# Performance work log

Hardware: AMD Instinct MI355X
Metric: run time of the kernel (lower is better)

The kernel has to match this reference:

```python
import jax, jax.numpy as jnp
import numpy as np

MB = 512          # mini_batch_size from init
BETA = 0.5        # RKHSMatrixOptimizer beta
N_SIGMAS = 50     # forward calls sigma_optimizer.step(..., 50)
EPS = 1e-6        # epsilon added to eigenvalues


def _pdist2(a):
    # squared Euclidean pairwise distances, matches torch.cdist(a, a)**2
    sq = jnp.sum(a * a, axis=1)
    d2 = sq[:, None] + sq[None, :] - 2.0 * (a @ a.T)
    return jnp.maximum(d2, 0.0)


def _rbf(d2, sigma):
    return jnp.exp(-d2 / (sigma ** 2))


def _entropy(A):
    # matrix-based Renyi entropy: eigh, +eps, -sum(w log2 w)
    w = jnp.linalg.eigvalsh(A) + EPS
    return -jnp.sum(w * jnp.log2(w))


def _joint_entropy(Ax, Ay):
    aux = Ax * Ay
    return _entropy(aux / jnp.trace(aux))


def _mi(Ax, Ay):
    return _entropy(Ax) + _entropy(Ay) - _joint_entropy(Ax, Ay)


def setup_inputs() -> dict:
    key = jax.random.key(0)
    k1, k2, k3 = jax.random.split(key, 3)
    x = jax.random.normal(k1, (4096, 8192), dtype=jnp.float32)
    inp = jax.random.normal(k2, (4096, 3, 32, 32), dtype=jnp.float32)
    label = jax.random.uniform(k3, (4096, 10), dtype=jnp.float32)
    return {"x": x, "input": inp, "label": label}


def reference(x, input, label):
    xf = x.reshape(x.shape[0], -1)
    inpf = input.reshape(input.shape[0], -1)
    n_batches = xf.shape[0] // MB

    sigma = None
    Ixt, Ity = [], []
    for b in range(n_batches):
        sl = slice(b * MB, (b + 1) * MB)
        xb, ib, lb = xf[sl], inpf[sl], label[sl]
        n = xb.shape[0]

        # label kernel Ky = RBF(label_batch, 0.1)
        Ky = _rbf(_pdist2(lb), 0.1)

        # sigma search: compute pairwise distances ONCE, broadcast over 50 sigmas
        d2 = _pdist2(xb)
        d = jnp.sqrt(d2)
        mean_d = jnp.sum(d) / jnp.maximum(jnp.sum(d2 > 0), 1)  # mean of nonzero dists
        start = 0.1 * mean_d
        step = (10.0 * mean_d - start) / N_SIGMAS
        sigmas = start + step * jnp.arange(N_SIGMAS, dtype=jnp.float32)  # np.arange equiv
        Ks = jnp.exp(-d2[None, :, :] / (sigmas[:, None, None] ** 2))  # [50, n, n]
        num = jnp.sum(Ks * Ky[None], axis=(1, 2))
        den = jnp.sqrt(jnp.sum(Ks * Ks, axis=(1, 2))) * jnp.linalg.norm(Ky)
        loss = num / den  # kernel alignment
        sigma_t = sigmas[jnp.argmax(loss)]
        sigma = sigma_t if sigma is None else BETA * sigma + (1.0 - BETA) * sigma_t

        # normalized Gram matrices (tensorRBFMatrix divides by batch size)
        A = _rbf(d2, sigma) / n
        Ay = Ky / n
        Ax = _rbf(_pdist2(ib), 8.0) / n

        Ixt.append(_mi(Ax, A))
        Ity.append(_mi(A, Ay))

    Ixt_mean = jnp.mean(jnp.stack(Ixt))
    Ity_mean = jnp.mean(jnp.stack(Ity))
    # torch forward returns x unchanged; MI values are stored as side effects.
    return x, Ixt_mean, Ity_mean
```

## Files before the change

kernel.cpp:

```cpp
#include <hip/hip_runtime.h>
#include <hip/hip_bf16.h>
#include <math.h>


#define NBATCH 8
#define MBS    512
#define DXX    8192
#define DII    3072
#define NSIG   50
#define NN     262144
#define NTOT   ((size_t)33554432)

#define I_SUMD  0
#define I_KYF   8
#define I_SIGMA 24
#define I_ENT   32
#define I_NUM   96
#define I_DEN   512
#define I_AX2   912
#define I_A2    920
#define I_JX2   928
#define I_JY2   936

typedef __attribute__((ext_vector_type(8))) short bf16x8;
typedef __attribute__((ext_vector_type(4))) float f32x4;

__device__ __forceinline__ size_t slotOf(int b, int m) {
  return ((size_t)(b * 5 + m)) * (size_t)NN;
}

__device__ __forceinline__ short f2b(float f) {
  __hip_bfloat16 h = __float2bfloat16(f);
  return *(short*)&h;
}

__device__ __forceinline__ ushort4 cvt4(float4 a) {
  ushort4 v;
  v.x = (ushort)f2b(a.x); v.y = (ushort)f2b(a.y);
  v.z = (ushort)f2b(a.z); v.w = (ushort)f2b(a.w);
  return v;
}

__device__ __forceinline__ double n4(float4 a) {
  return (double)a.x * a.x + (double)a.y * a.y + (double)a.z * a.z + (double)a.w * a.w;
}

__device__ __forceinline__ void nt_store4(float4 v, float4* p) {
  f32x4 w = {v.x, v.y, v.z, v.w};
  __builtin_nontemporal_store(w, (f32x4*)p);
}

__global__ void k_copy(const float4* __restrict__ src, float4* __restrict__ dst, size_t n4) {
  size_t i = (size_t)blockIdx.x * blockDim.x + threadIdx.x;
  size_t stride = (size_t)gridDim.x * blockDim.x;
  for (; i < n4; i += stride) dst[i] = src[i];
}

__global__ __launch_bounds__(256) void k_prep(
    const float4* __restrict__ x4, float4* __restrict__ xcopy, int docopy,
    const float* __restrict__ inp, const float* __restrict__ lab,
    ushort* __restrict__ xbf, ushort* __restrict__ inpbf,
    float* __restrict__ nrmx, float* __restrict__ nrmi,
    float* __restrict__ eig, double* __restrict__ scal)
{
  __shared__ double red[256];
  int bid = blockIdx.x, t = threadIdx.x;

  if (bid < 4096) {
    int row = bid;
    const float4* p4 = x4 + (size_t)row * 2048;
    float4 f0 = p4[t];
    float4 f1 = p4[t + 256];
    float4 f2 = p4[t + 512];
    float4 f3 = p4[t + 768];
    float4 f4 = p4[t + 1024];
    float4 f5 = p4[t + 1280];
    float4 f6 = p4[t + 1536];
    float4 f7 = p4[t + 1792];
    if (docopy) {
      float4* q4 = xcopy + (size_t)row * 2048;
      nt_store4(f0, q4 + t);
      nt_store4(f1, q4 + t + 256);
      nt_store4(f2, q4 + t + 512);
      nt_store4(f3, q4 + t + 768);
      nt_store4(f4, q4 + t + 1024);
      nt_store4(f5, q4 + t + 1280);
      nt_store4(f6, q4 + t + 1536);
      nt_store4(f7, q4 + t + 1792);
    }
    ushort4* o4 = (ushort4*)(xbf + (size_t)row * 8192);
    o4[t]        = cvt4(f0);
    o4[t + 256]  = cvt4(f1);
    o4[t + 512]  = cvt4(f2);
    o4[t + 768]  = cvt4(f3);
    o4[t + 1024] = cvt4(f4);
    o4[t + 1280] = cvt4(f5);
    o4[t + 1536] = cvt4(f6);
    o4[t + 1792] = cvt4(f7);
    double s = n4(f0) + n4(f1) + n4(f2) + n4(f3) + n4(f4) + n4(f5) + n4(f6) + n4(f7);
    red[t] = s; __syncthreads();
    for (int o2 = 128; o2 > 0; o2 >>= 1) {
      if (t < o2) red[t] += red[t + o2];
      __syncthreads();
    }
    if (t == 0) nrmx[row] = (float)red[0];
    return;
  }

  if (bid < 6144) {
    int p = bid - 4096;
    const float4* src4 = (const float4*)inp + (size_t)p * 768;
    ushort4* dst4 = (ushort4*)inpbf + (size_t)p * 768;
    float4 g0 = src4[t];
    float4 g1 = src4[t + 256];
    float4 g2 = src4[t + 512];
    dst4[t]       = cvt4(g0);
    dst4[t + 256] = cvt4(g1);
    dst4[t + 512] = cvt4(g2);
    double s0 = n4(g0), s1 = n4(g2);
    double sm = n4(g1);
    if (t < 128) s0 += sm; else s1 += sm;
    red[t] = s0; __syncthreads();
    for (int o = 128; o > 0; o >>= 1) { if (t < o) red[t] += red[t + o]; __syncthreads(); }
    if (t == 0) nrmi[2 * p] = (float)red[0];
    __syncthreads();
    red[t] = s1; __syncthreads();
    for (int o = 128; o > 0; o >>= 1) { if (t < o) red[t] += red[t + o]; __syncthreads(); }
    if (t == 0) nrmi[2 * p + 1] = (float)red[0];
    return;
  }

  int idx = bid - 6144;
  int b = idx >> 8, xb = idx & 255;
  int e0 = xb * 1024 + t * 4;
  int i = e0 >> 9;
  const float* L = lab + (size_t)b * MBS * 10;
  float4 out;
  double s = 0.0;
#pragma unroll
  for (int u = 0; u < 4; u++) {
    int j = (e0 & 511) + u;
    float d2 = 0.0f;
#pragma unroll
    for (int d = 0; d < 10; d++) { float dd = L[i * 10 + d] - L[j * 10 + d]; d2 += dd * dd; }
    float ky = __expf(-d2 * 100.0f);
    ((float*)&out)[u] = ky * (1.0f / 512.0f);
    s += (double)ky * ky;
  }
  *(float4*)&eig[slotOf(b, 2) + e0] = out;
  red[t] = s; __syncthreads();
  for (int o = 128; o > 0; o >>= 1) { if (t < o) red[t] += red[t + o]; __syncthreads(); }
  if (t == 0) atomicAdd(&scal[I_KYF + b], red[0]);
}

#define LSTR 72
#define LGKM0_BAR                                                             \
  do {                                                                        \
    asm volatile("s_waitcnt lgkmcnt(0)" ::: "memory");                        \
    __builtin_amdgcn_s_barrier();                                             \
    __builtin_amdgcn_sched_barrier(0);                                        \
  } while (0)

#define LOAD_SET(A0, A1, B0, B1, K0)                                          \
  do {                                                                        \
    A0 = *(const bf16x8*)&srcA0[K0];                                          \
    A1 = *(const bf16x8*)&srcA1[K0];                                          \
    B0 = *(const bf16x8*)&srcB0[K0];                                          \
    B1 = *(const bf16x8*)&srcB1[K0];                                          \
  } while (0)

#define WRITE_LDS(BUF, A0, A1, B0, B1)                                        \
  do {                                                                        \
    *(bf16x8*)&As[BUF][rr * LSTR + cc] = A0;                                  \
    *(bf16x8*)&As[BUF][(32 + rr) * LSTR + cc] = A1;                           \
    *(bf16x8*)&Bs[BUF][rr * LSTR + cc] = B0;                                  \
    *(bf16x8*)&Bs[BUF][(32 + rr) * LSTR + cc] = B1;                           \
  } while (0)

#define MFMA_PHASE(BUF)                                                       \
  do {                                                                        \
    _Pragma("unroll")                                                         \
    for (int ks = 0; ks < 2; ks++) {                                          \
      bf16x8 af0 = *(const bf16x8*)&As[BUF][(wr + l15) * LSTR + ks * 32 + l4 * 8];          \
      bf16x8 af1 = *(const bf16x8*)&As[BUF][(wr + 16 + l15) * LSTR + ks * 32 + l4 * 8];     \
      bf16x8 bg0 = *(const bf16x8*)&Bs[BUF][(wc + l15) * LSTR + ks * 32 + l4 * 8];          \
      bf16x8 bg1 = *(const bf16x8*)&Bs[BUF][(wc + 16 + l15) * LSTR + ks * 32 + l4 * 8];     \
      acc00 = __builtin_amdgcn_mfma_f32_16x16x32_bf16(af0, bg0, acc00, 0, 0, 0);            \
      acc01 = __builtin_amdgcn_mfma_f32_16x16x32_bf16(af0, bg1, acc01, 0, 0, 0);            \
      acc10 = __builtin_amdgcn_mfma_f32_16x16x32_bf16(af1, bg0, acc10, 0, 0, 0);            \
      acc11 = __builtin_amdgcn_mfma_f32_16x16x32_bf16(af1, bg1, acc11, 0, 0, 0);            \
    }                                                                         \
  } while (0)

__global__ __launch_bounds__(256) void k_gemm2(
    const ushort* __restrict__ xbf, const ushort* __restrict__ inpbf,
    const float* __restrict__ nrmx, const float* __restrict__ nrmi,
    float* __restrict__ eig, double* __restrict__ scal,
    unsigned long long* __restrict__ cnt)
{
  int id = blockIdx.x;
  int b = id & 7;
  int tm = id >> 3;
  int mode = (tm >= 36) ? 1 : 0;
  int t = tm - mode * 36;
  int bx = 0;
#pragma unroll
  for (int r = 1; r < 8; r++) if (t >= (r * (r + 1)) / 2) bx = r;
  int by = t - (bx * (bx + 1)) / 2;
  bool diag = (bx == by);
  int D = mode ? DII : DXX;
  const ushort* src = (mode ? inpbf : xbf) + (size_t)b * MBS * D;
  const float* nb = (mode ? nrmi : nrmx) + b * MBS;
  int row0 = bx * 64, col0 = by * 64;

  __shared__ ushort As[2][64 * LSTR];
  __shared__ ushort Bs[2][64 * LSTR];
  __shared__ double redd[256];
  __shared__ unsigned redi[256];

  int tid = threadIdx.x;
  int lane = tid & 63, w = tid >> 6;
  int wr = (w >> 1) * 32, wc = (w & 1) * 32;
  int l15 = lane & 15, l4 = lane >> 4;

  f32x4 acc00 = {0.f, 0.f, 0.f, 0.f}, acc01 = {0.f, 0.f, 0.f, 0.f};
  f32x4 acc10 = {0.f, 0.f, 0.f, 0.f}, acc11 = {0.f, 0.f, 0.f, 0.f};

  int rr = tid >> 3;
  int cc = (tid & 7) * 8;

  const ushort* srcA0 = src + (size_t)(row0 + rr) * D + cc;
  const ushort* srcA1 = src + (size_t)(row0 + 32 + rr) * D + cc;
  const ushort* srcB0 = src + (size_t)(col0 + rr) * D + cc;
  const ushort* srcB1 = src + (size_t)(col0 + 32 + rr) * D + cc;

  bf16x8 pa0, pa1, pb0, pb1;
  bf16x8 qa0, qa1, qb0, qb1;

  LOAD_SET(pa0, pa1, pb0, pb1, 0);
  LOAD_SET(qa0, qa1, qb0, qb1, 64);

  int nk = D >> 6;
  for (int k = 0; k < nk; k += 2) {
    WRITE_LDS(0, pa0, pa1, pb0, pb1);
    if (k + 2 < nk) LOAD_SET(pa0, pa1, pb0, pb1, (k + 2) << 6);
    LGKM0_BAR;
    MFMA_PHASE(0);
    WRITE_LDS(1, qa0, qa1, qb0, qb1);
    if (k + 3 < nk) LOAD_SET(qa0, qa1, qb0, qb1, (k + 3) << 6);
    LGKM0_BAR;
    MFMA_PHASE(1);
  }

  float* dst = eig + slotOf(b, mode ? 0 : 1);
  double lsum = 0.0; unsigned lcnt = 0;
#define EPI(ACC, M, N)                                                        \
  do {                                                                        \
    int gr = row0 + wr + (M) * 16 + l4 * 4;                                   \
    int gc = col0 + wc + (N) * 16 + l15;                                      \
    float nj = nb[gc];                                                        \
    _Pragma("unroll")                                                         \
    for (int v = 0; v < 4; v++) {                                             \
      int gi = gr + v;                                                        \
      float d2 = nb[gi] + nj - 2.0f * ACC[v];                                 \
      d2 = fmaxf(d2, 0.0f);                                                   \
      if (gi == gc) d2 = 0.0f;                                                \
      float val;                                                              \
      if (mode == 0) {                                                        \
        val = d2;                                                             \
        if (d2 > 0.0f) { lsum += (double)sqrtf(d2); lcnt++; }                 \
      } else {                                                                \
        val = __expf(-d2 * (1.0f / 64.0f)) * (1.0f / 512.0f);                 \
        lsum += (double)val * val;                                            \
      }                                                                       \
      dst[(size_t)gi * MBS + gc] = val;                                       \
      if (!diag) dst[(size_t)gc * MBS + gi] = val;                            \
    }                                                                         \
  } while (0)
  EPI(acc00, 0, 0); EPI(acc01, 0, 1); EPI(acc10, 1, 0); EPI(acc11, 1, 1);
#undef EPI

  if (!diag) { lsum *= 2.0; lcnt *= 2; }
  __syncthreads();
  redd[tid] = lsum; redi[tid] = lcnt; __syncthreads();
  for (int o = 128; o > 0; o >>= 1) {
    if (tid < o) { redd[tid] += redd[tid + o]; redi[tid] += redi[tid + o]; }
    __syncthreads();
  }
  if (tid == 0) {
    if (mode == 0) {
      atomicAdd(&scal[I_SUMD + b], redd[0]);
      atomicAdd(&cnt[b], (unsigned long long)redi[0]);
    } else {
      atomicAdd(&scal[I_AX2 + b], redd[0]);
    }
  }
}

__global__ __launch_bounds__(256) void k_loss(const float* __restrict__ eig,
                                              double* __restrict__ scal,
                                              const unsigned long long* __restrict__ cnt,
                                              unsigned* __restrict__ done) {
  int b = blockIdx.z, g = blockIdx.y;
  double c = (double)cnt[b]; if (c < 1.0) c = 1.0;
  float md = (float)(scal[I_SUMD + b] / c);
  const float4* d2p = (const float4*)(eig + slotOf(b, 1));
  const float4* ayp = (const float4*)(eig + slotOf(b, 2));
  float inv[25], ln[25], ld[25];
#pragma unroll
  for (int i = 0; i < 25; i++) {
    float sg = md * (0.1f + 0.198f * (float)(g * 25 + i));
    inv[i] = 1.0f / (sg * sg);
    ln[i] = 0.0f; ld[i] = 0.0f;
  }
  int base = blockIdx.x * 2048 + threadIdx.x;
#pragma unroll
  for (int l = 0; l < 8; l++) {
    float4 d2v = d2p[base + l * 256];
    float4 ayv = ayp[base + l * 256];
#pragma unroll
    for (int u = 0; u < 4; u++) {
      float d2 = ((const float*)&d2v)[u];
      float ay = ((const float*)&ayv)[u];
#pragma unroll
      for (int i = 0; i < 25; i++) {
        float kk = __expf(-d2 * inv[i]);
        ln[i] = fmaf(kk, ay, ln[i]);
        ld[i] = fmaf(kk, kk, ld[i]);
      }
    }
  }
#pragma unroll
  for (int i = 0; i < 25; i++) {
    float a = ln[i], d = ld[i];
    for (int o = 32; o > 0; o >>= 1) {
      a += __shfl_down(a, o, 64);
      d += __shfl_down(d, o, 64);
    }
    if ((threadIdx.x & 63) == 0) {
      atomicAdd(&scal[I_NUM + b * NSIG + g * 25 + i], (double)a * 512.0);
      atomicAdd(&scal[I_DEN + b * NSIG + g * 25 + i], (double)d);
    }
  }
  __syncthreads();
  if (threadIdx.x == 0) {
    __threadfence();
    unsigned r = atomicAdd(done, 1u);
    if (r == 32 * 2 * NBATCH - 1) {
      __threadfence();
      double sigma = 0.0;
      for (int bb = 0; bb < NBATCH; bb++) {
        double cc2 = (double)cnt[bb]; if (cc2 < 1.0) cc2 = 1.0;
        double mdd = scal[I_SUMD + bb] / cc2;
        double kyf = sqrt(scal[I_KYF + bb]);
        double best = -1.0; int bi = 0;
        for (int s = 0; s < NSIG; s++) {
          double num = scal[I_NUM + bb * NSIG + s];
          double den = sqrt(scal[I_DEN + bb * NSIG + s]) * kyf;
          double loss = num / den;
          if (loss > best) { best = loss; bi = s; }
        }
        double st = mdd * (0.1 + 0.198 * (double)bi);
        sigma = (bb == 0) ? st : 0.5 * sigma + 0.5 * st;
        scal[I_SIGMA + bb] = sigma;
      }
    }
  }
}

__global__ __launch_bounds__(256) void k_aj(float* __restrict__ eig,
                                            double* __restrict__ scal) {
  int b = blockIdx.y;
  float sg = (float)scal[I_SIGMA + b];
  float inv = 1.0f / (sg * sg);
  float* A        = eig + slotOf(b, 1);
  const float* AX = eig + slotOf(b, 0);
  const float* AY = eig + slotOf(b, 2);
  float* J1       = eig + slotOf(b, 3);
  float* J2       = eig + slotOf(b, 4);
  double s1 = 0.0, s2 = 0.0, s3 = 0.0;
  size_t base = (size_t)blockIdx.x * 2048 + (size_t)threadIdx.x * 8;
#pragma unroll
  for (int h = 0; h < 2; h++) {
    size_t e = base + h * 4;
    float4 d2v = *(float4*)&A[e];
    float4 axv = *(const float4*)&AX[e];
    float4 ayv = *(const float4*)&AY[e];
    float4 av, j1v, j2v;
#pragma unroll
    for (int u = 0; u < 4; u++) {
      float a = __expf(-((const float*)&d2v)[u] * inv) * (1.0f / 512.0f);
      float j1 = ((const float*)&axv)[u] * a;
      float j2 = a * ((const float*)&ayv)[u];
      ((float*)&av)[u] = a; ((float*)&j1v)[u] = j1; ((float*)&j2v)[u] = j2;
      s1 += (double)a * a; s2 += (double)j1 * j1; s3 += (double)j2 * j2;
    }
    *(float4*)&A[e] = av;
    *(float4*)&J1[e] = j1v;
    *(float4*)&J2[e] = j2v;
  }
  __shared__ double r1[256], r2[256], r3[256];
  r1[threadIdx.x] = s1; r2[threadIdx.x] = s2; r3[threadIdx.x] = s3;
  __syncthreads();
  for (int o = 128; o > 0; o >>= 1) {
    if (threadIdx.x < o) {
      r1[threadIdx.x] += r1[threadIdx.x + o];
      r2[threadIdx.x] += r2[threadIdx.x + o];
      r3[threadIdx.x] += r3[threadIdx.x + o];
    }
    __syncthreads();
  }
  if (threadIdx.x == 0) {
    atomicAdd(&scal[I_A2 + b], r1[0]);
    atomicAdd(&scal[I_JX2 + b], r2[0]);
    atomicAdd(&scal[I_JY2 + b], r3[0]);
  }
}

__global__ __launch_bounds__(512) void k_eigen(float* __restrict__ eig,
                                               double* __restrict__ scal,
                                               unsigned* __restrict__ done,
                                               float* __restrict__ out) {
  int blk = blockIdx.x; int b = blk / 5, m = blk % 5;
  int t = threadIdx.x;
  double off2, scale0;
  if (m == 0)      { off2 = scal[I_AX2 + b] - (1.0 / 512.0);              scale0 = 1.0; }
  else if (m == 1) { off2 = scal[I_A2 + b]  - (1.0 / 512.0);              scale0 = 1.0; }
  else if (m == 2) { off2 = (scal[I_KYF + b] - 512.0) * (1.0 / 262144.0); scale0 = 1.0; }
  else if (m == 3) { off2 = scal[I_JX2 + b] - 7.450580596923828125e-9;    scale0 = 512.0; }
  else             { off2 = scal[I_JY2 + b] - 7.450580596923828125e-9;    scale0 = 512.0; }

  if (off2 * scale0 * scale0 <= 1e-8) {
    if (t == 0) {
      double diagv = (m >= 3) ? (1.0 / 262144.0) : (1.0 / 512.0);
      double wv = diagv * scale0 + 1e-6;
      scal[I_ENT + b * 5 + m] = -512.0 * wv * log2(wv);
    }
  } else {
    float* M = eig + slotOf(b, m);
    __shared__ double red[512];
    __shared__ float csA[256], csB[256];
    __shared__ int anyrot;
    __shared__ double sh_scale, sh_off2;

    red[t] = (double)M[(size_t)t * 513]; __syncthreads();
    for (int o = 256; o > 0; o >>= 1) { if (t < o) red[t] += red[t + o]; __syncthreads(); }
    if (t == 0) { double trace = red[0]; sh_scale = (m >= 3) ? 1.0 / trace : 1.0; }
    __syncthreads();
    double scale = sh_scale;

    for (int sweep = 0; sweep < 30; sweep++) {
      double c2 = 0.0;
      for (int i = 0; i < 512; i++) {
        if (i != t) { float v = M[(size_t)i * 512 + t]; c2 += (double)v * v; }
      }
      red[t] = c2; __syncthreads();
      for (int o = 256; o > 0; o >>= 1) { if (t < o) red[t] += red[t + o]; __syncthreads(); }
      if (t == 0) sh_off2 = red[0];
      __syncthreads();
      if (sh_off2 * scale * scale <= 1e-8) break;

      for (int r = 0; r < 511; r++) {
        if (t == 0) anyrot = 0;
        __syncthreads();
        if (t < 256) {
          int p, q;
          if (t == 0) { p = 511; q = r; }
          else { p = (r + t) % 511; q = (r + 511 - t) % 511; }
          float app = M[(size_t)p * 512 + p];
          float aqq = M[(size_t)q * 512 + q];
          float apq = M[(size_t)p * 512 + q];
          float c = 1.0f, sr = 0.0f;
          if (fabsf(apq) > 1e-12f) {
            float th = (aqq - app) / (2.0f * apq);
            float tt = ((th >= 0.0f) ? 1.0f : -1.0f) / (fabsf(th) + sqrtf(1.0f + th * th));
            c = 1.0f / sqrtf(1.0f + tt * tt);
            sr = tt * c;
            anyrot = 1;
          }
          csA[t] = c; csB[t] = sr;
        }
        __syncthreads();
        if (anyrot) {
          int pair = t >> 1, half = t & 1;
          float c = csA[pair], sr = csB[pair];
          int p, q;
          if (pair == 0) { p = 511; q = r; }
          else { p = (r + pair) % 511; q = (r + 511 - pair) % 511; }
          if (sr != 0.0f) {
            size_t rp = (size_t)p * 512, rq = (size_t)q * 512;
            int j0 = half * 256;
            for (int j = j0; j < j0 + 256; j++) {
              float xx = M[rp + j], yy = M[rq + j];
              M[rp + j] = c * xx - sr * yy;
              M[rq + j] = sr * xx + c * yy;
            }
          }
          __syncthreads();
          if (sr != 0.0f) {
            int j0 = half * 256;
            for (int j = j0; j < j0 + 256; j++) {
              float xx = M[(size_t)j * 512 + p], yy = M[(size_t)j * 512 + q];
              M[(size_t)j * 512 + p] = c * xx - sr * yy;
              M[(size_t)j * 512 + q] = sr * xx + c * yy;
            }
          }
        }
        __syncthreads();
      }
    }

    double wv = (double)M[(size_t)t * 513] * scale + 1e-6;
    red[t] = -wv * log2(wv); __syncthreads();
    for (int o = 256; o > 0; o >>= 1) { if (t < o) red[t] += red[t + o]; __syncthreads(); }
    if (t == 0) scal[I_ENT + b * 5 + m] = red[0];
  }

  __syncthreads();
  if (t == 0) {
    __threadfence();
    unsigned r = atomicAdd(done, 1u);
    if (r == 39) {
      __threadfence();
      double ixt = 0.0, ity = 0.0;
      for (int bb = 0; bb < NBATCH; bb++) {
        const double* E = &scal[I_ENT + bb * 5];
        ixt += E[0] + E[1] - E[3];
        ity += E[1] + E[2] - E[4];
      }
      out[NTOT]     = (float)(ixt / 8.0);
      out[NTOT + 1] = (float)(ity / 8.0);
    }
  }
}

extern "C" void kernel_launch(void* const* d_in, const int* in_sizes, int n_in,
                              void* d_out, int out_size, void* d_ws, size_t ws_size,
                              hipStream_t stream) {
  const float* x   = (const float*)d_in[0];
  const float* inp = (const float*)d_in[1];
  const float* lab = (const float*)d_in[2];
  float* out = (float*)d_out;

  char* ws = (char*)d_ws;
  double* scal = (double*)ws;
  unsigned long long* cnt = (unsigned long long*)(ws + 7552);
  unsigned* done_loss = (unsigned*)(ws + 7616);
  unsigned* done_eig  = (unsigned*)(ws + 7620);
  float* nrmx = (float*)(ws + 7680);
  float* nrmi = (float*)(ws + 24064);

  const size_t EIG_OFF = 65536;
  bool big = ws_size >= EIG_OFF + 134217728ULL;
  char* base = big ? (ws + EIG_OFF) : (char*)d_out;
  float* eig = (float*)base;
  ushort* xbf = (ushort*)(base + 41943040);
  ushort* inpbf = (ushort*)(base + 109051904);

  hipMemsetAsync(ws, 0, 7624, stream);

  k_prep<<<8192, 256, 0, stream>>>((const float4*)x, (float4*)d_out, big ? 1 : 0,
                                   inp, lab, xbf, inpbf, nrmx, nrmi, eig, scal);
  k_gemm2<<<576, 256, 0, stream>>>(xbf, inpbf, nrmx, nrmi, eig, scal, cnt);
  k_loss<<<dim3(32, 2, NBATCH), 256, 0, stream>>>(eig, scal, cnt, done_loss);
  k_aj<<<dim3(128, NBATCH), 256, 0, stream>>>(eig, scal);
  k_eigen<<<40, 512, 0, stream>>>(eig, scal, done_eig, out);
  if (!big) {
    k_copy<<<2048, 256, 0, stream>>>((const float4*)x, (float4*)d_out, NTOT / 4);
  }
}
```

Before: 280.2 us.

## Move output copy of x from prep kernel into extra GEMM blocks

The 128 MB passthrough copy of x to the output moves out of k_prep and into 2048 extra blocks appended to the k_gemm2 grid, which use nontemporal loads and stores. The aim is to overlap the bandwidth-bound copy with the compute-bound GEMM blocks, and to make k_prep lighter by dropping its store stream. Sched barriers are also added in k_prep so all loads issue before the converts and stores. The risk is that the copy blocks compete with GEMM blocks for CUs and memory bandwidth, and x is now read from DRAM twice instead of once.

Measured after the change: 281.7 us. About the same (+0.5%).

```diff
diff --git a/kernel.cpp b/kernel.cpp
--- a/kernel.cpp
+++ b/kernel.cpp
@@ -10,6 +10,7 @@
 #define NSIG   50
 #define NN     262144
 #define NTOT   ((size_t)33554432)
+#define NGEMM  576
 
 #define I_SUMD  0
 #define I_KYF   8
@@ -45,11 +46,6 @@
   return (double)a.x * a.x + (double)a.y * a.y + (double)a.z * a.z + (double)a.w * a.w;
 }
 
-__device__ __forceinline__ void nt_store4(float4 v, float4* p) {
-  f32x4 w = {v.x, v.y, v.z, v.w};
-  __builtin_nontemporal_store(w, (f32x4*)p);
-}
-
 __global__ void k_copy(const float4* __restrict__ src, float4* __restrict__ dst, size_t n4) {
   size_t i = (size_t)blockIdx.x * blockDim.x + threadIdx.x;
   size_t stride = (size_t)gridDim.x * blockDim.x;
@@ -57,7 +53,7 @@
 }
 
 __global__ __launch_bounds__(256) void k_prep(
-    const float4* __restrict__ x4, float4* __restrict__ xcopy, int docopy,
+    const float4* __restrict__ x4,
     const float* __restrict__ inp, const float* __restrict__ lab,
     ushort* __restrict__ xbf, ushort* __restrict__ inpbf,
     float* __restrict__ nrmx, float* __restrict__ nrmi,
@@ -77,17 +73,7 @@
     float4 f5 = p4[t + 1280];
     float4 f6 = p4[t + 1536];
     float4 f7 = p4[t + 1792];
-    if (docopy) {
-      float4* q4 = xcopy + (size_t)row * 2048;
-      nt_store4(f0, q4 + t);
-      nt_store4(f1, q4 + t + 256);
-      nt_store4(f2, q4 + t + 512);
-      nt_store4(f3, q4 + t + 768);
-      nt_store4(f4, q4 + t + 1024);
-      nt_store4(f5, q4 + t + 1280);
-      nt_store4(f6, q4 + t + 1536);
-      nt_store4(f7, q4 + t + 1792);
-    }
+    __builtin_amdgcn_sched_barrier(0);
     ushort4* o4 = (ushort4*)(xbf + (size_t)row * 8192);
     o4[t]        = cvt4(f0);
     o4[t + 256]  = cvt4(f1);
@@ -114,6 +100,7 @@
     float4 g0 = src4[t];
     float4 g1 = src4[t + 256];
     float4 g2 = src4[t + 512];
+    __builtin_amdgcn_sched_barrier(0);
     dst4[t]       = cvt4(g0);
     dst4[t + 256] = cvt4(g1);
     dst4[t + 512] = cvt4(g2);
@@ -196,9 +183,38 @@
     const ushort* __restrict__ xbf, const ushort* __restrict__ inpbf,
     const float* __restrict__ nrmx, const float* __restrict__ nrmi,
     float* __restrict__ eig, double* __restrict__ scal,
-    unsigned long long* __restrict__ cnt)
+    unsigned long long* __restrict__ cnt,
+    const f32x4* __restrict__ xsrc, f32x4* __restrict__ xdst)
 {
   int id = blockIdx.x;
+  int tid = threadIdx.x;
+
+  if (id >= NGEMM) {
+    size_t base = (size_t)(id - NGEMM) * 4096 + tid;
+#pragma unroll
+    for (int h = 0; h < 2; h++) {
+      size_t o = base + (size_t)h * 2048;
+      f32x4 c0 = __builtin_nontemporal_load(xsrc + o);
+      f32x4 c1 = __builtin_nontemporal_load(xsrc + o + 256);
+      f32x4 c2 = __builtin_nontemporal_load(xsrc + o + 512);
+      f32x4 c3 = __builtin_nontemporal_load(xsrc + o + 768);
+      f32x4 c4 = __builtin_nontemporal_load(xsrc + o + 1024);
+      f32x4 c5 = __builtin_nontemporal_load(xsrc + o + 1280);
+      f32x4 c6 = __builtin_nontemporal_load(xsrc + o + 1536);
+      f32x4 c7 = __builtin_nontemporal_load(xsrc + o + 1792);
+      __builtin_amdgcn_sched_barrier(0);
+      __builtin_nontemporal_store(c0, xdst + o);
+      __builtin_nontemporal_store(c1, xdst + o + 256);
+      __builtin_nontemporal_store(c2, xdst + o + 512);
+      __builtin_nontemporal_store(c3, xdst + o + 768);
+      __builtin_nontemporal_store(c4, xdst + o + 1024);
+      __builtin_nontemporal_store(c5, xdst + o + 1280);
+      __builtin_nontemporal_store(c6, xdst + o + 1536);
+      __builtin_nontemporal_store(c7, xdst + o + 1792);
+    }
+    return;
+  }
+
   int b = id & 7;
   int tm = id >> 3;
   int mode = (tm >= 36) ? 1 : 0;
@@ -218,7 +234,6 @@
   __shared__ double redd[256];
   __shared__ unsigned redi[256];
 
-  int tid = threadIdx.x;
   int lane = tid & 63, w = tid >> 6;
   int wr = (w >> 1) * 32, wc = (w & 1) * 32;
   int l15 = lane & 15, l4 = lane >> 4;
@@ -559,9 +574,11 @@
 
   hipMemsetAsync(ws, 0, 7624, stream);
 
-  k_prep<<<8192, 256, 0, stream>>>((const float4*)x, (float4*)d_out, big ? 1 : 0,
-                                   inp, lab, xbf, inpbf, nrmx, nrmi, eig, scal);
-  k_gemm2<<<576, 256, 0, stream>>>(xbf, inpbf, nrmx, nrmi, eig, scal, cnt);
+  k_prep<<<8192, 256, 0, stream>>>((const float4*)x, inp, lab,
+                                   xbf, inpbf, nrmx, nrmi, eig, scal);
+  int ncopy = big ? 2048 : 0;
+  k_gemm2<<<NGEMM + ncopy, 256, 0, stream>>>(xbf, inpbf, nrmx, nrmi, eig, scal, cnt,
+                                             (const f32x4*)x, (f32x4*)d_out);
   k_loss<<<dim3(32, 2, NBATCH), 256, 0, stream>>>(eig, scal, cnt, done_loss);
   k_aj<<<dim3(128, NBATCH), 256, 0, stream>>>(eig, scal);
   k_eigen<<<40, 512, 0, stream>>>(eig, scal, done_eig, out);
```
